# Kernel optimization log

Measured on AMD Instinct MI355X. Metric: run time of the kernel, lower is better.

Reference implementation:

```python
import jax, jax.numpy as jnp
import numpy as np

DIM = 128
HID = 256
NB = 2048      # number of sets (batches)
NTOT = 32768   # total elements across all sets
NMAX = 32      # cap on decoded set size (padded/masked)
VAL_MID = (DIM + HID) // 2    # 192, build_mlp midmult=1.0
SIZE_MID = (HID + 1) // 2     # 128
DEC_MID = (HID + DIM) // 2    # 192


def mish(x):
    return x * jnp.tanh(jax.nn.softplus(x))


def layernorm(x, g, b):
    m = x.mean(-1, keepdims=True)
    v = x.var(-1, keepdims=True)
    return (x - m) / jnp.sqrt(v + 1e-5) * g + b


def _lin_init(key, fan_in, fan_out):
    return jax.random.normal(key, (fan_in, fan_out), jnp.float32) / np.sqrt(fan_in)


def setup_inputs() -> dict:
    key = jax.random.key(0)
    ks = jax.random.split(key, 16)
    x = jax.random.normal(ks[0], (NTOT, DIM), jnp.float32)
    batch = jnp.sort(jax.random.randint(ks[1], (NTOT,), 0, NB)).astype(jnp.int64)
    return {
        "x": x, "batch": batch,
        # encoder rank (Linear(dim,1))
        "rank_w": _lin_init(ks[2], DIM, 1)[:, 0], "rank_b": jnp.zeros((), jnp.float32),
        # encoder val_net: Linear -> LayerNorm -> Mish -> Linear
        "val_w1": _lin_init(ks[3], DIM, VAL_MID), "val_b1": jnp.zeros((VAL_MID,), jnp.float32),
        "val_ln_g": jnp.ones((VAL_MID,), jnp.float32), "val_ln_b": jnp.zeros((VAL_MID,), jnp.float32),
        "val_w2": _lin_init(ks[4], VAL_MID, HID), "val_b2": jnp.zeros((HID,), jnp.float32),
        # shared cardinality Linear(1, hidden)
        "card_w": _lin_init(ks[5], 1, HID), "card_b": jnp.zeros((HID,), jnp.float32),
        # decoder size_pred: Linear -> LayerNorm -> Mish -> Linear
        "size_w1": _lin_init(ks[6], HID, SIZE_MID), "size_b1": jnp.zeros((SIZE_MID,), jnp.float32),
        "size_ln_g": jnp.ones((SIZE_MID,), jnp.float32), "size_ln_b": jnp.zeros((SIZE_MID,), jnp.float32),
        "size_w2": _lin_init(ks[7], SIZE_MID, 1), "size_b2": jnp.zeros((1,), jnp.float32),
        # decoder mlp: Linear -> Mish -> Linear (no layernorm)
        "dec_w1": _lin_init(ks[8], HID, DEC_MID), "dec_b1": jnp.zeros((DEC_MID,), jnp.float32),
        "dec_w2": _lin_init(ks[9], DEC_MID, DIM), "dec_b2": jnp.zeros((DIM,), jnp.float32),
    }


def reference(x, batch, rank_w, rank_b, val_w1, val_b1, val_ln_g, val_ln_b,
              val_w2, val_b2, card_w, card_b, size_w1, size_b1, size_ln_g,
              size_ln_b, size_w2, size_b2, dec_w1, dec_b1, dec_w2, dec_b2):
    batch = batch.astype(jnp.int32)
    t = jnp.linspace(0.0, 1.0, HID)

    # ---- encoder ----
    n = jax.ops.segment_sum(jnp.ones((NTOT,), jnp.float32), batch, num_segments=NB)
    n_i = n.astype(jnp.int32)
    mag = x @ rank_w + rank_b                       # [NTOT]
    # sort within each contiguous batch segment: stable lexsort (batch primary)
    order = jnp.lexsort((mag, batch))
    xs = x[order]
    seg_start = jnp.cumsum(n_i) - n_i               # per-set start offset
    k = (jnp.arange(NTOT, dtype=jnp.int32) - seg_start[batch]).astype(jnp.float32)
    keys = jnp.exp(1j * t[None, :] * k[:, None] * 8.0)            # [NTOT,HID] complex
    h = mish(layernorm(xs @ val_w1 + val_b1, val_ln_g, val_ln_b)) @ val_w2 + val_b2
    y = h.astype(jnp.complex64) * keys
    z_el = jax.ops.segment_sum(y, batch, num_segments=NB)         # [NB,HID] complex
    n_enc = n[:, None] @ card_w + card_b
    z = z_el + n_enc

    # ---- decoder ----
    h2 = mish(layernorm(z.real @ size_w1 + size_b1, size_ln_g, size_ln_b)) @ size_w2 + size_b2
    n_pred = jnp.maximum(jnp.round(h2[:, 0]), 0.0)                # [NB]
    n_pred_i = jnp.minimum(n_pred.astype(jnp.int32), NMAX)
    n_enc2 = n_pred[:, None] @ card_w + card_b
    zc = z - n_enc2
    kk = jnp.arange(NMAX, dtype=jnp.float32)
    keys2 = jnp.exp(1j * t[None, :] * kk[:, None] * 8.0)          # [NMAX,HID]
    zp = zc[:, None, :] * keys2[None, :, :]                       # [NB,NMAX,HID] complex
    xr = mish(zp.real @ dec_w1 + dec_b1) @ dec_w2 + dec_b2        # [NB,NMAX,DIM]
    mask = jnp.arange(NMAX)[None, :] < n_pred_i[:, None]          # [NB,NMAX]
    xr = jnp.where(mask[:, :, None], xr, 0.0)
    return xr, mask, n_pred_i
```

## Files before the change

### kernel.cpp

```cpp
#include <hip/hip_runtime.h>
#include <math.h>

#define DIMX 128
#define HIDX 256
#define NBX 2048
#define NTOTX 32768
#define NMAXX 32
#define VMID 192
#define SMID 128
#define DMID 192

#define EROWS 64
#define SP 65
#define NSEGMAX 128

__device__ __forceinline__ float mishf(float v) {
    if (v > 20.0f) return v;
    float u = expf(v);
    float t = u * (u + 2.0f);
    return v * (t / (t + 2.0f));
}

__global__ __launch_bounds__(1024, 2) void k_enc(const float* __restrict__ x,
    const float* __restrict__ rw, const float* __restrict__ rb,
    const float* __restrict__ w1, const float* __restrict__ b1,
    const float* __restrict__ g1, const float* __restrict__ be1,
    const float* __restrict__ w2, const float* __restrict__ b2,
    float* __restrict__ h, float* __restrict__ mag) {
    __shared__ __align__(16) float sbuf[VMID * SP];
    __shared__ float red[1024];
    __shared__ float red2[1024];
    int tid = threadIdx.x;
    int r = tid & 63;
    int tg = tid >> 6;
    int rowbase = blockIdx.x * EROWS;

#pragma unroll
    for (int it = 0; it < 2; it++) {
        int f4 = it * 1024 + tid;
        int rr = f4 >> 5, kq = f4 & 31;
        float4 v = ((const float4*)x)[(size_t)(rowbase + rr) * 32 + kq];
        sbuf[(4 * kq + 0) * SP + rr] = v.x;
        sbuf[(4 * kq + 1) * SP + rr] = v.y;
        sbuf[(4 * kq + 2) * SP + rr] = v.z;
        sbuf[(4 * kq + 3) * SP + rr] = v.w;
    }
    __syncthreads();

    if (tid < 64) {
        float s = 0.0f;
        for (int k = 0; k < DIMX; k++) s += sbuf[k * SP + tid] * rw[k];
        mag[rowbase + tid] = s + rb[0];
    }

    int cb1 = __builtin_amdgcn_readfirstlane(tg * 12);
    float acc[12];
#pragma unroll
    for (int j = 0; j < 12; j++) acc[j] = 0.0f;
#pragma unroll 4
    for (int k = 0; k < DIMX; k++) {
        float xv = sbuf[k * SP + r];
        const float* wr = w1 + k * VMID + cb1;
#pragma unroll
        for (int j = 0; j < 12; j++) acc[j] += wr[j] * xv;
    }

    float part = 0.0f;
#pragma unroll
    for (int j = 0; j < 12; j++) { acc[j] += b1[cb1 + j]; part += acc[j]; }
    red[tg * 64 + r] = part;
    __syncthreads();
    float mean = 0.0f;
#pragma unroll
    for (int q = 0; q < 16; q++) mean += red[q * 64 + r];
    mean *= (1.0f / 192.0f);
    float vpart = 0.0f;
#pragma unroll
    for (int j = 0; j < 12; j++) { acc[j] -= mean; vpart += acc[j] * acc[j]; }
    red2[tg * 64 + r] = vpart;
    __syncthreads();
    float var = 0.0f;
#pragma unroll
    for (int q = 0; q < 16; q++) var += red2[q * 64 + r];
    var *= (1.0f / 192.0f);
    float inv = 1.0f / sqrtf(var + 1e-5f);
#pragma unroll
    for (int j = 0; j < 12; j++)
        acc[j] = mishf(acc[j] * inv * g1[cb1 + j] + be1[cb1 + j]);
    __syncthreads();
#pragma unroll
    for (int j = 0; j < 12; j++) sbuf[(cb1 + j) * SP + r] = acc[j];
    __syncthreads();

    int cb2 = __builtin_amdgcn_readfirstlane(tg * 16);
    float acc2[16];
#pragma unroll
    for (int j = 0; j < 16; j++) acc2[j] = 0.0f;
#pragma unroll 4
    for (int k = 0; k < VMID; k++) {
        float av = sbuf[k * SP + r];
        const float* wr = w2 + k * HIDX + cb2;
#pragma unroll
        for (int j = 0; j < 16; j++) acc2[j] += wr[j] * av;
    }
    float* hp = h + (size_t)(rowbase + r) * HIDX + cb2;
#pragma unroll
    for (int q = 0; q < 4; q++) {
        float4 v;
        v.x = acc2[4 * q + 0] + b2[cb2 + 4 * q + 0];
        v.y = acc2[4 * q + 1] + b2[cb2 + 4 * q + 1];
        v.z = acc2[4 * q + 2] + b2[cb2 + 4 * q + 2];
        v.w = acc2[4 * q + 3] + b2[cb2 + 4 * q + 3];
        ((float4*)hp)[q] = v;
    }
}

__global__ __launch_bounds__(256) void k_z(const float* __restrict__ h,
    const int* __restrict__ batch, const float* __restrict__ mag,
    const float* __restrict__ cw, const float* __restrict__ cb,
    float* __restrict__ zre, float* __restrict__ zim) {
    __shared__ float magL[NSEGMAX];
    __shared__ int   ordL[NSEGMAX];
    __shared__ int   shs, shn;
    int b = blockIdx.x, j = threadIdx.x;
    if (j == 0) {
        int lo = 0, hi = NTOTX;
        while (lo < hi) { int m = (lo + hi) >> 1; if (batch[m] < b) lo = m + 1; else hi = m; }
        int stt = lo;
        hi = NTOTX;
        while (lo < hi) { int m = (lo + hi) >> 1; if (batch[m] <= b) lo = m + 1; else hi = m; }
        shs = stt; shn = lo - stt;
    }
    __syncthreads();
    int s = shs, n_true = shn;
    int n = (n_true < NSEGMAX) ? n_true : NSEGMAX;
    if (j < n) magL[j] = mag[s + j];
    __syncthreads();
    if (j < n) {
        float mi = magL[j];
        int rk = 0;
        for (int q = 0; q < n; q++) {
            float mq = magL[q];
            rk += (mq < mi) || (mq == mi && q < j);
        }
        ordL[rk] = s + j;
    }
    __syncthreads();

    float t = (float)j * (1.0f / 255.0f);
    float zr = 0.f, zi = 0.f;
    int p = 0;
    for (; p + 1 < n; p += 2) {
        int e0 = ordL[p], e1 = ordL[p + 1];
        float hv0 = h[(size_t)e0 * HIDX + j];
        float hv1 = h[(size_t)e1 * HIDX + j];
        float sv0, cv0, sv1, cv1;
        sincosf((t * (float)p) * 8.0f, &sv0, &cv0);
        sincosf((t * (float)(p + 1)) * 8.0f, &sv1, &cv1);
        zr += hv0 * cv0; zi += hv0 * sv0;
        zr += hv1 * cv1; zi += hv1 * sv1;
    }
    if (p < n) {
        int e = ordL[p];
        float hv = h[(size_t)e * HIDX + j];
        float sv, cv;
        sincosf((t * (float)p) * 8.0f, &sv, &cv);
        zr += hv * cv; zi += hv * sv;
    }
    float nf = (float)n_true;
    zre[(size_t)b * HIDX + j] = zr + nf * cw[j] + cb[j];
    zim[(size_t)b * HIDX + j] = zi;
}

__global__ __launch_bounds__(256) void k_size(const float* __restrict__ zre,
    const float* __restrict__ cw, const float* __restrict__ cb,
    const float* __restrict__ sw1, const float* __restrict__ sb1,
    const float* __restrict__ sg, const float* __restrict__ sbe,
    const float* __restrict__ sw2, const float* __restrict__ sb2,
    float* __restrict__ zcre, float* __restrict__ out_mask,
    float* __restrict__ out_np, int* __restrict__ npredi) {
    __shared__ float zs[8][HIDX];
    __shared__ float rA[16], rB[16], rC[16];
    __shared__ float snpf[8];
    int tid = threadIdx.x;
    int b0 = blockIdx.x * 8;
#pragma unroll
    for (int it = 0; it < 8; it++) {
        int idx = it * 256 + tid;
        zs[idx >> 8][idx & 255] = zre[(size_t)(b0 + (idx >> 8)) * HIDX + (idx & 255)];
    }
    __syncthreads();

    int g = tid >> 7;
    int j = tid & 127;
    int wv = (tid >> 6) & 1;
    float acc[4];
    float vb1 = sb1[j];
#pragma unroll
    for (int q = 0; q < 4; q++) acc[q] = vb1;
    for (int k = 0; k < HIDX; k++) {
        float w = sw1[k * SMID + j];
#pragma unroll
        for (int q = 0; q < 4; q++) acc[q] += zs[g * 4 + q][k] * w;
    }
#pragma unroll
    for (int q = 0; q < 4; q++) {
        float sa = acc[q];
#pragma unroll
        for (int off = 32; off; off >>= 1) sa += __shfl_xor(sa, off, 64);
        if ((tid & 63) == 0) rA[(g * 2 + wv) * 4 + q] = sa;
    }
    __syncthreads();
    float d[4];
#pragma unroll
    for (int q = 0; q < 4; q++) {
        float mean = (rA[(g * 2) * 4 + q] + rA[(g * 2 + 1) * 4 + q]) / 128.0f;
        d[q] = acc[q] - mean;
        float qq = d[q] * d[q];
#pragma unroll
        for (int off = 32; off; off >>= 1) qq += __shfl_xor(qq, off, 64);
        if ((tid & 63) == 0) rB[(g * 2 + wv) * 4 + q] = qq;
    }
    __syncthreads();
    float gj = sg[j], bej = sbe[j], w2j = sw2[j];
#pragma unroll
    for (int q = 0; q < 4; q++) {
        float var = (rB[(g * 2) * 4 + q] + rB[(g * 2 + 1) * 4 + q]) / 128.0f;
        float lv = d[q] * (1.0f / sqrtf(var + 1e-5f)) * gj + bej;
        float p2 = mishf(lv) * w2j;
#pragma unroll
        for (int off = 32; off; off >>= 1) p2 += __shfl_xor(p2, off, 64);
        if ((tid & 63) == 0) rC[(g * 2 + wv) * 4 + q] = p2;
    }
    __syncthreads();
    if (tid < 8) {
        int q = tid & 3, gg = tid >> 2;
        float h2 = rC[(gg * 2) * 4 + q] + rC[(gg * 2 + 1) * 4 + q] + sb2[0];
        float npf = fmaxf(rintf(h2), 0.0f);
        int npi = min((int)npf, NMAXX);
        snpf[tid] = npf;
        out_np[b0 + tid] = (float)npi;
        npredi[b0 + tid] = npi;
    }
    __syncthreads();
#pragma unroll
    for (int it = 0; it < 8; it++) {
        int idx = it * 256 + tid;
        int bi = idx >> 8, jj = idx & 255;
        zcre[(size_t)(b0 + bi) * HIDX + jj] = zs[bi][jj] - (snpf[bi] * cw[jj] + cb[jj]);
    }
    {
        int bi = tid >> 5, m = tid & 31;
        out_mask[(b0 + bi) * NMAXX + m] = (m < ((int)fminf(snpf[bi], 32.0f))) ? 1.0f : 0.0f;
    }
}

__global__ __launch_bounds__(256) void k_dec(const float* __restrict__ zcre,
    const float* __restrict__ zim, const int* __restrict__ npredi,
    const float* __restrict__ w1, const float* __restrict__ b1,
    const float* __restrict__ w2, const float* __restrict__ b2,
    float* __restrict__ xr) {
    int m = blockIdx.x, b = blockIdx.y;
    int tid = threadIdx.x;
    size_t row = (size_t)b * NMAXX + m;
    if (m >= npredi[b]) {
        if (tid < DIMX) xr[row * DIMX + tid] = 0.0f;
        return;
    }
    __shared__ float zp[HIDX];
    __shared__ float a[DMID];
    {
        float t = (float)tid * (1.0f / 255.0f);
        float sv, cv;
        sincosf((t * (float)m) * 8.0f, &sv, &cv);
        zp[tid] = zcre[(size_t)b * HIDX + tid] * cv - zim[(size_t)b * HIDX + tid] * sv;
    }
    __syncthreads();
    if (tid < DMID) {
        float v = b1[tid];
#pragma unroll 4
        for (int k = 0; k < HIDX; k++) v += zp[k] * w1[k * DMID + tid];
        a[tid] = mishf(v);
    }
    __syncthreads();
    if (tid < DIMX) {
        float v = b2[tid];
#pragma unroll 4
        for (int k = 0; k < DMID; k++) v += a[k] * w2[k * DIMX + tid];
        xr[row * DIMX + tid] = v;
    }
}

extern "C" void kernel_launch(void* const* d_in, const int* in_sizes, int n_in,
                              void* d_out, int out_size, void* d_ws, size_t ws_size,
                              hipStream_t stream) {
    const float* x      = (const float*)d_in[0];
    const int*   batch  = (const int*)d_in[1];
    const float* rank_w = (const float*)d_in[2];
    const float* rank_b = (const float*)d_in[3];
    const float* vw1    = (const float*)d_in[4];
    const float* vb1    = (const float*)d_in[5];
    const float* vlg    = (const float*)d_in[6];
    const float* vlb    = (const float*)d_in[7];
    const float* vw2    = (const float*)d_in[8];
    const float* vb2    = (const float*)d_in[9];
    const float* cw     = (const float*)d_in[10];
    const float* cb     = (const float*)d_in[11];
    const float* sw1    = (const float*)d_in[12];
    const float* sb1    = (const float*)d_in[13];
    const float* slg    = (const float*)d_in[14];
    const float* slb    = (const float*)d_in[15];
    const float* sw2    = (const float*)d_in[16];
    const float* sb2    = (const float*)d_in[17];
    const float* dw1    = (const float*)d_in[18];
    const float* db1    = (const float*)d_in[19];
    const float* dw2    = (const float*)d_in[20];
    const float* db2    = (const float*)d_in[21];

    char* ws = (char*)d_ws;
    size_t off = 0;
    auto alloc = [&](size_t bytes) {
        void* p = ws + off;
        off += (bytes + 255) & ~(size_t)255;
        return p;
    };
    float* mag  = (float*)alloc((size_t)NTOTX * 4);
    float* zre  = (float*)alloc((size_t)NBX * HIDX * 4);
    float* zim  = (float*)alloc((size_t)NBX * HIDX * 4);
    float* zcre = (float*)alloc((size_t)NBX * HIDX * 4);
    int*   npi  = (int*)alloc((size_t)NBX * 4);
    float* h    = (float*)alloc((size_t)NTOTX * HIDX * 4);

    float* out_xr   = (float*)d_out;
    float* out_mask = out_xr + (size_t)NBX * NMAXX * DIMX;
    float* out_np   = out_mask + (size_t)NBX * NMAXX;

    hipLaunchKernelGGL(k_enc,  dim3(NTOTX / EROWS), dim3(1024), 0, stream,
                       x, rank_w, rank_b, vw1, vb1, vlg, vlb, vw2, vb2, h, mag);
    hipLaunchKernelGGL(k_z,    dim3(NBX), dim3(HIDX), 0, stream,
                       h, batch, mag, cw, cb, zre, zim);
    hipLaunchKernelGGL(k_size, dim3(NBX / 8), dim3(256), 0, stream,
                       zre, cw, cb, sw1, sb1, slg, slb, sw2, sb2,
                       zcre, out_mask, out_np, npi);
    hipLaunchKernelGGL(k_dec,  dim3(NMAXX, NBX), dim3(256), 0, stream,
                       zcre, zim, npi, dw1, db1, dw2, db2, out_xr);
    (void)in_sizes; (void)n_in; (void)out_size; (void)ws_size;
}
```

Baseline: 149.6 us.

## Retile encoder MLP with register-blocked rows and pre-interleaved float4 weights

```diff
diff --git a/kernel.cpp b/kernel.cpp
--- a/kernel.cpp
+++ b/kernel.cpp
@@ -10,8 +10,8 @@
 #define SMID 128
 #define DMID 192
 
-#define EROWS 64
-#define SP 65
+#define EROWS 32
+#define SP 34
 #define NSEGMAX 128
 
 __device__ __forceinline__ float mishf(float v) {
@@ -21,97 +21,142 @@
     return v * (t / (t + 2.0f));
 }
 
-__global__ __launch_bounds__(1024, 2) void k_enc(const float* __restrict__ x,
+__global__ void k_wt(const float* __restrict__ w1, const float* __restrict__ w2,
+                     float* __restrict__ wI1, float* __restrict__ wI2) {
+    int i = blockIdx.x * blockDim.x + threadIdx.x;
+    if (i < DIMX * VMID) {
+        int k = i / VMID, c = i % VMID;
+        wI1[((k >> 2) * VMID + c) * 4 + (k & 3)] = w1[i];
+    }
+    int i2 = i - DIMX * VMID;
+    if (i2 >= 0 && i2 < VMID * HIDX) {
+        int k = i2 / HIDX, c = i2 % HIDX;
+        wI2[((k >> 2) * HIDX + c) * 4 + (k & 3)] = w2[i2];
+    }
+}
+
+__global__ __launch_bounds__(256, 4) void k_enc(const float* __restrict__ x,
     const float* __restrict__ rw, const float* __restrict__ rb,
-    const float* __restrict__ w1, const float* __restrict__ b1,
+    const float4* __restrict__ wI1, const float* __restrict__ b1,
     const float* __restrict__ g1, const float* __restrict__ be1,
-    const float* __restrict__ w2, const float* __restrict__ b2,
+    const float4* __restrict__ wI2, const float* __restrict__ b2,
     float* __restrict__ h, float* __restrict__ mag) {
-    __shared__ __align__(16) float sbuf[VMID * SP];
-    __shared__ float red[1024];
-    __shared__ float red2[1024];
+    __shared__ __align__(16) float sT[VMID * SP];
     int tid = threadIdx.x;
-    int r = tid & 63;
-    int tg = tid >> 6;
     int rowbase = blockIdx.x * EROWS;
 
 #pragma unroll
-    for (int it = 0; it < 2; it++) {
-        int f4 = it * 1024 + tid;
-        int rr = f4 >> 5, kq = f4 & 31;
-        float4 v = ((const float4*)x)[(size_t)(rowbase + rr) * 32 + kq];
-        sbuf[(4 * kq + 0) * SP + rr] = v.x;
-        sbuf[(4 * kq + 1) * SP + rr] = v.y;
-        sbuf[(4 * kq + 2) * SP + rr] = v.z;
-        sbuf[(4 * kq + 3) * SP + rr] = v.w;
-    }
-    __syncthreads();
-
-    if (tid < 64) {
+    for (int it = 0; it < 4; it++) {
+        int idx = it * 256 + tid;
+        int r = idx >> 5, kq = idx & 31;
+        float4 v = ((const float4*)x)[(size_t)(rowbase + r) * 32 + kq];
+        sT[(4 * kq + 0) * SP + r] = v.x;
+        sT[(4 * kq + 1) * SP + r] = v.y;
+        sT[(4 * kq + 2) * SP + r] = v.z;
+        sT[(4 * kq + 3) * SP + r] = v.w;
+    }
+    __syncthreads();
+
+    if (tid < EROWS) {
         float s = 0.0f;
-        for (int k = 0; k < DIMX; k++) s += sbuf[k * SP + tid] * rw[k];
+        for (int k = 0; k < DIMX; k++) s += sT[k * SP + tid] * rw[k];
         mag[rowbase + tid] = s + rb[0];
     }
 
-    int cb1 = __builtin_amdgcn_readfirstlane(tg * 12);
-    float acc[12];
-#pragma unroll
-    for (int j = 0; j < 12; j++) acc[j] = 0.0f;
-#pragma unroll 4
-    for (int k = 0; k < DIMX; k++) {
-        float xv = sbuf[k * SP + r];
-        const float* wr = w1 + k * VMID + cb1;
-#pragma unroll
-        for (int j = 0; j < 12; j++) acc[j] += wr[j] * xv;
-    }
-
-    float part = 0.0f;
-#pragma unroll
-    for (int j = 0; j < 12; j++) { acc[j] += b1[cb1 + j]; part += acc[j]; }
-    red[tg * 64 + r] = part;
-    __syncthreads();
-    float mean = 0.0f;
-#pragma unroll
-    for (int q = 0; q < 16; q++) mean += red[q * 64 + r];
-    mean *= (1.0f / 192.0f);
-    float vpart = 0.0f;
-#pragma unroll
-    for (int j = 0; j < 12; j++) { acc[j] -= mean; vpart += acc[j] * acc[j]; }
-    red2[tg * 64 + r] = vpart;
-    __syncthreads();
-    float var = 0.0f;
-#pragma unroll
-    for (int q = 0; q < 16; q++) var += red2[q * 64 + r];
-    var *= (1.0f / 192.0f);
-    float inv = 1.0f / sqrtf(var + 1e-5f);
-#pragma unroll
-    for (int j = 0; j < 12; j++)
-        acc[j] = mishf(acc[j] * inv * g1[cb1 + j] + be1[cb1 + j]);
-    __syncthreads();
-#pragma unroll
-    for (int j = 0; j < 12; j++) sbuf[(cb1 + j) * SP + r] = acc[j];
-    __syncthreads();
-
-    int cb2 = __builtin_amdgcn_readfirstlane(tg * 16);
-    float acc2[16];
-#pragma unroll
-    for (int j = 0; j < 16; j++) acc2[j] = 0.0f;
-#pragma unroll 4
-    for (int k = 0; k < VMID; k++) {
-        float av = sbuf[k * SP + r];
-        const float* wr = w2 + k * HIDX + cb2;
-#pragma unroll
-        for (int j = 0; j < 16; j++) acc2[j] += wr[j] * av;
-    }
-    float* hp = h + (size_t)(rowbase + r) * HIDX + cb2;
-#pragma unroll
-    for (int q = 0; q < 4; q++) {
-        float4 v;
-        v.x = acc2[4 * q + 0] + b2[cb2 + 4 * q + 0];
-        v.y = acc2[4 * q + 1] + b2[cb2 + 4 * q + 1];
-        v.z = acc2[4 * q + 2] + b2[cb2 + 4 * q + 2];
-        v.w = acc2[4 * q + 3] + b2[cb2 + 4 * q + 3];
-        ((float4*)hp)[q] = v;
+    int c = tid & 63;
+    int rg = tid >> 6;
+    int r0 = rg * 8;
+
+    float a0[8], a1[8], a2[8];
+#pragma unroll
+    for (int i = 0; i < 8; i++) { a0[i] = 0.f; a1[i] = 0.f; a2[i] = 0.f; }
+    const float4* w1g = wI1 + c;
+#pragma unroll 2
+    for (int kg = 0; kg < DIMX / 4; kg++) {
+        float4 wa = w1g[kg * VMID];
+        float4 wb = w1g[kg * VMID + 64];
+        float4 wc = w1g[kg * VMID + 128];
+        const float waA[4] = {wa.x, wa.y, wa.z, wa.w};
+        const float wbA[4] = {wb.x, wb.y, wb.z, wb.w};
+        const float wcA[4] = {wc.x, wc.y, wc.z, wc.w};
+#pragma unroll
+        for (int kk = 0; kk < 4; kk++) {
+            const float2* xp = (const float2*)&sT[(4 * kg + kk) * SP + r0];
+            float2 t0 = xp[0], t1 = xp[1], t2 = xp[2], t3 = xp[3];
+            float xv[8] = {t0.x, t0.y, t1.x, t1.y, t2.x, t2.y, t3.x, t3.y};
+#pragma unroll
+            for (int i = 0; i < 8; i++) {
+                a0[i] += waA[kk] * xv[i];
+                a1[i] += wbA[kk] * xv[i];
+                a2[i] += wcA[kk] * xv[i];
+            }
+        }
+    }
+
+    float b1a = b1[c], b1b = b1[c + 64], b1c = b1[c + 128];
+    float g1a = g1[c], g1b = g1[c + 64], g1c = g1[c + 128];
+    float e1a = be1[c], e1b = be1[c + 64], e1c = be1[c + 128];
+#pragma unroll
+    for (int i = 0; i < 8; i++) {
+        float v0 = a0[i] + b1a, v1 = a1[i] + b1b, v2 = a2[i] + b1c;
+        float s = v0 + v1 + v2;
+#pragma unroll
+        for (int off = 32; off; off >>= 1) s += __shfl_xor(s, off, 64);
+        float mean = s / 192.0f;
+        float d0 = v0 - mean, d1 = v1 - mean, d2 = v2 - mean;
+        float q = d0 * d0 + d1 * d1 + d2 * d2;
+#pragma unroll
+        for (int off = 32; off; off >>= 1) q += __shfl_xor(q, off, 64);
+        float inv = 1.0f / sqrtf(q / 192.0f + 1e-5f);
+        a0[i] = mishf(d0 * inv * g1a + e1a);
+        a1[i] = mishf(d1 * inv * g1b + e1b);
+        a2[i] = mishf(d2 * inv * g1c + e1c);
+    }
+    __syncthreads();
+#pragma unroll
+    for (int i = 0; i < 8; i++) {
+        sT[c * SP + r0 + i]          = a0[i];
+        sT[(c + 64) * SP + r0 + i]   = a1[i];
+        sT[(c + 128) * SP + r0 + i]  = a2[i];
+    }
+    __syncthreads();
+
+    float c0[8], c1[8], c2[8], c3[8];
+#pragma unroll
+    for (int i = 0; i < 8; i++) { c0[i] = 0.f; c1[i] = 0.f; c2[i] = 0.f; c3[i] = 0.f; }
+    const float4* w2g = wI2 + c;
+#pragma unroll 2
+    for (int kg = 0; kg < VMID / 4; kg++) {
+        float4 wa = w2g[kg * HIDX];
+        float4 wb = w2g[kg * HIDX + 64];
+        float4 wc = w2g[kg * HIDX + 128];
+        float4 wd = w2g[kg * HIDX + 192];
+        const float waA[4] = {wa.x, wa.y, wa.z, wa.w};
+        const float wbA[4] = {wb.x, wb.y, wb.z, wb.w};
+        const float wcA[4] = {wc.x, wc.y, wc.z, wc.w};
+        const float wdA[4] = {wd.x, wd.y, wd.z, wd.w};
+#pragma unroll
+        for (int kk = 0; kk < 4; kk++) {
+            const float2* ap = (const float2*)&sT[(4 * kg + kk) * SP + r0];
+            float2 t0 = ap[0], t1 = ap[1], t2 = ap[2], t3 = ap[3];
+            float av[8] = {t0.x, t0.y, t1.x, t1.y, t2.x, t2.y, t3.x, t3.y};
+#pragma unroll
+            for (int i = 0; i < 8; i++) {
+                c0[i] += waA[kk] * av[i];
+                c1[i] += wbA[kk] * av[i];
+                c2[i] += wcA[kk] * av[i];
+                c3[i] += wdA[kk] * av[i];
+            }
+        }
+    }
+    float b2a = b2[c], b2b = b2[c + 64], b2c = b2[c + 128], b2d = b2[c + 192];
+#pragma unroll
+    for (int i = 0; i < 8; i++) {
+        size_t row = (size_t)(rowbase + r0 + i);
+        h[row * HIDX + c]        = c0[i] + b2a;
+        h[row * HIDX + c + 64]   = c1[i] + b2b;
+        h[row * HIDX + c + 128]  = c2[i] + b2c;
+        h[row * HIDX + c + 192]  = c3[i] + b2d;
     }
 }
 
@@ -329,14 +374,19 @@
     float* zim  = (float*)alloc((size_t)NBX * HIDX * 4);
     float* zcre = (float*)alloc((size_t)NBX * HIDX * 4);
     int*   npi  = (int*)alloc((size_t)NBX * 4);
+    float* wI1  = (float*)alloc((size_t)DIMX * VMID * 4);
+    float* wI2  = (float*)alloc((size_t)VMID * HIDX * 4);
     float* h    = (float*)alloc((size_t)NTOTX * HIDX * 4);
 
     float* out_xr   = (float*)d_out;
     float* out_mask = out_xr + (size_t)NBX * NMAXX * DIMX;
     float* out_np   = out_mask + (size_t)NBX * NMAXX;
 
-    hipLaunchKernelGGL(k_enc,  dim3(NTOTX / EROWS), dim3(1024), 0, stream,
-                       x, rank_w, rank_b, vw1, vb1, vlg, vlb, vw2, vb2, h, mag);
+    hipLaunchKernelGGL(k_wt,   dim3((DIMX * VMID + VMID * HIDX + 255) / 256), dim3(256), 0, stream,
+                       vw1, vw2, wI1, wI2);
+    hipLaunchKernelGGL(k_enc,  dim3(NTOTX / EROWS), dim3(256), 0, stream,
+                       x, rank_w, rank_b, (const float4*)wI1, vb1, vlg, vlb,
+                       (const float4*)wI2, vb2, h, mag);
     hipLaunchKernelGGL(k_z,    dim3(NBX), dim3(HIDX), 0, stream,
                        h, batch, mag, cw, cb, zre, zim);
     hipLaunchKernelGGL(k_size, dim3(NBX / 8), dim3(256), 0, stream,
```

After: 155.2 us. 3.7% more time.
